# Kernel tuning notes

Hardware: AMD Instinct MI355X
Metric: run time of the kernel (lower is better)

## Reference

```python
import jax, jax.numpy as jnp
import numpy as np

D_MODEL = 2048
NUM_HEADS = 16
HEAD_DIM = D_MODEL // NUM_HEADS
BATCH = 2
SEQ = 2048


def setup_inputs() -> dict:
    key = jax.random.key(0)
    ks = jax.random.split(key, 5)
    s = 1.0 / np.sqrt(D_MODEL)
    return {
        "x": jax.random.normal(ks[0], (BATCH, SEQ, D_MODEL), dtype=jnp.float32),
        "Wq": jax.random.normal(ks[1], (D_MODEL, D_MODEL), dtype=jnp.float32) * s,
        "Wk": jax.random.normal(ks[2], (D_MODEL, D_MODEL), dtype=jnp.float32) * s,
        "Wv": jax.random.normal(ks[3], (D_MODEL, D_MODEL), dtype=jnp.float32) * s,
        "Wo": jax.random.normal(ks[4], (D_MODEL, D_MODEL), dtype=jnp.float32) * s,
    }


def reference(x, Wq, Wk, Wv, Wo):
    B, S, D = x.shape
    H, Dh = NUM_HEADS, HEAD_DIM
    # nn.Linear(bias=False): y = x @ W.T ; split_heads is a plain view (no transpose!)
    Q = (x @ Wq.T).reshape(B, H, S, Dh)
    K = (x @ Wk.T).reshape(B, H, S, Dh)
    V = (x @ Wv.T).reshape(B, H, S, Dh)
    # scores scaled by head_dim (NOT sqrt) — faithful to source
    scores = jnp.einsum("bhqd,bhkd->bhqk", Q, K) / jnp.float32(Dh)
    causal_mask = jnp.triu(jnp.ones((S, S), dtype=bool), k=1)  # True above diagonal
    scores = jnp.where(causal_mask, -jnp.inf, scores)
    attn = jax.nn.softmax(scores, axis=-1)
    out = jnp.einsum("bhqk,bhkd->bhqd", attn, V)  # [B,H,S,Dh]
    out = out.transpose(0, 2, 1, 3).reshape(B, S, D)  # merge DOES transpose
    return out @ Wo.T
```

## Files before the change

kernel.cpp:

```cpp
#include <hip/hip_runtime.h>
#include <hip/hip_bf16.h>

using bf16 = __hip_bfloat16;
typedef __attribute__((ext_vector_type(8))) short bf16x8;
typedef __attribute__((ext_vector_type(4))) float f32x4;

#define DEVI __device__ __forceinline__

constexpr int Bn = 2, Sn = 2048, Dn = 2048, Hn = 16, DHn = 128;
constexpr int Mn = Bn * Sn;

DEVI void gload_lds16(const bf16* g, bf16* l) {
  __builtin_amdgcn_global_load_lds(
      (__attribute__((address_space(1))) void*)g,
      (__attribute__((address_space(3))) void*)l,
      16, 0, 0);
}

__global__ __launch_bounds__(256) void cvt_all_k(const float* __restrict__ x,
                                                 const float* __restrict__ wq,
                                                 const float* __restrict__ wk,
                                                 const float* __restrict__ wv,
                                                 const float* __restrict__ wo,
                                                 bf16* __restrict__ xb,
                                                 bf16* __restrict__ wb) {
  const int which = blockIdx.y;
  const float* src;
  bf16* dst;
  int n8;
  if (which == 0) { src = x;  dst = xb; n8 = Mn * Dn / 8; }
  else {
    src = (which == 1) ? wq : (which == 2) ? wk : (which == 3) ? wv : wo;
    dst = wb + (size_t)(which - 1) * Dn * Dn;
    n8 = Dn * Dn / 8;
  }
  for (int i = blockIdx.x * 256 + threadIdx.x; i < n8; i += gridDim.x * 256) {
    const float4* p = (const float4*)src + (size_t)i * 2;
    float4 a = p[0], b = p[1];
    union { bf16 h[8]; bf16x8 v; } u;
    u.h[0] = __float2bfloat16(a.x); u.h[1] = __float2bfloat16(a.y);
    u.h[2] = __float2bfloat16(a.z); u.h[3] = __float2bfloat16(a.w);
    u.h[4] = __float2bfloat16(b.x); u.h[5] = __float2bfloat16(b.y);
    u.h[6] = __float2bfloat16(b.z); u.h[7] = __float2bfloat16(b.w);
    *((bf16x8*)dst + i) = u.v;
  }
}

template <int OUTF32, int NTOT, int NMAT, int MW>
__global__ __launch_bounds__(256, 2) void gemm3s(const bf16* __restrict__ A,
                                                 const bf16* __restrict__ W,
                                                 void* __restrict__ Cv) {
  constexpr int K = 2048, NT = K / 32;
  constexpr int BM = MW * 32;
  constexpr int SLOT = (BM + 128) * 32;
  __shared__ bf16 smem[3 * SLOT];

  constexpr int MT = Mn / BM;
  const int nwg = NTOT * MT;
  const int orig = blockIdx.x;
  const int wgid = (orig & 7) * (nwg >> 3) + (orig >> 3);
  const int bm = wgid / NTOT;
  const int bnn = wgid % NTOT;
  constexpr int nper = NTOT / NMAT;
  const int z = bnn / nper;
  const int col0 = (bnn % nper) * 128;

  const int t = threadIdx.x;
  const int wave = t >> 6, lane = t & 63;
  const int wm = wave >> 1, wn = wave & 1;
  const int lr = lane & 15, lg = lane >> 4;
  const int rch = ((lg ^ ((lr >> 1) & 3)) * 8);
  const int srow = t >> 2;
  const int sch = (t & 3) ^ ((t >> 3) & 3);

  const bf16* Ab = A + (size_t)(bm * BM + srow) * K + sch * 8;
  const bf16* Bb = W + (size_t)z * (2048 * 2048) +
                   (size_t)(col0 + srow) * K + sch * 8;

  auto stgA = [&](int slot, int kt, int u) {
    gload_lds16(Ab + (size_t)u * 64 * K + kt * 32,
                smem + slot * SLOT + u * 2048 + t * 8);
  };
  auto stgB = [&](int slot, int kt, int v) {
    gload_lds16(Bb + (size_t)v * 64 * K + kt * 32,
                smem + slot * SLOT + BM * 32 + v * 2048 + t * 8);
  };
  auto stage_tile = [&](int slot, int kt) {
#pragma unroll
    for (int u = 0; u < MW / 2; ++u) stgA(slot, kt, u);
    stgB(slot, kt, 0); stgB(slot, kt, 1);
  };

  f32x4 acc[MW][4];
  const f32x4 zf = {0.f, 0.f, 0.f, 0.f};
#pragma unroll
  for (int i = 0; i < MW; ++i)
#pragma unroll
    for (int j = 0; j < 4; ++j) acc[i][j] = zf;

  stage_tile(0, 0);
  stage_tile(1, 1);

  int slot = 0;
#pragma unroll 1
  for (int kt = 0; kt < NT; ++kt) {
    const bf16* sAb = smem + slot * SLOT;
    const bf16* sBb = sAb + BM * 32;

    if (kt == NT - 1)            asm volatile("s_waitcnt vmcnt(0)" ::: "memory");
    else if constexpr (MW == 8)  asm volatile("s_waitcnt vmcnt(6)" ::: "memory");
    else                         asm volatile("s_waitcnt vmcnt(4)" ::: "memory");
    __builtin_amdgcn_s_barrier();

    if (kt + 2 < NT) {
      int ps = slot + 2; if (ps >= 3) ps -= 3;
      stage_tile(ps, kt + 2);
    }

    bf16x8 bv[4], af[MW];
#pragma unroll
    for (int n = 0; n < 4; ++n)
      bv[n] = *(const bf16x8*)(sBb + (wn * 64 + n * 16 + lr) * 32 + rch);
#pragma unroll
    for (int i = 0; i < MW; ++i)
      af[i] = *(const bf16x8*)(sAb + (wm * (MW * 16) + i * 16 + lr) * 32 + rch);

    __builtin_amdgcn_s_setprio(1);
#pragma unroll
    for (int i = 0; i < MW; ++i)
#pragma unroll
      for (int n = 0; n < 4; ++n)
        acc[i][n] = __builtin_amdgcn_mfma_f32_16x16x32_bf16(af[i], bv[n], acc[i][n], 0, 0, 0);
    __builtin_amdgcn_s_setprio(0);

    slot = (slot == 2) ? 0 : slot + 1;
  }

  const int r0 = bm * BM + wm * (MW * 16), c0 = col0 + wn * 64;
#pragma unroll
  for (int mm = 0; mm < MW; ++mm)
#pragma unroll
    for (int nn = 0; nn < 4; ++nn) {
      const int rr = r0 + mm * 16 + lg * 4;
      const int cc = c0 + nn * 16 + lr;
#pragma unroll
      for (int r = 0; r < 4; ++r) {
        float v = acc[mm][nn][r];
        if (OUTF32) {
          ((float*)Cv)[(size_t)(rr + r) * 2048 + cc] = v;
        } else {
          bf16* C = (bf16*)Cv + (size_t)z * (Mn * 2048);
          C[(size_t)(rr + r) * 2048 + cc] = __float2bfloat16(v);
        }
      }
    }
}

__global__ __launch_bounds__(256, 2) void transpose_v(const bf16* __restrict__ V,
                                                      bf16* __restrict__ VT) {
  __shared__ bf16 tile[128 * 128];
  const int kt = blockIdx.x, bh = blockIdx.y;
  const bf16* Vh = V + (size_t)bh * (Sn * DHn);
  bf16* VTh = VT + (size_t)bh * (DHn * Sn);
  const int t = threadIdx.x;
  const int rr = t >> 4, cc = t & 15;
#pragma unroll
  for (int i = 0; i < 8; ++i) {
    int r = rr + i * 16;
    int ch = cc ^ ((r >> 3) & 7);
    *(bf16x8*)(tile + r * 128 + ch * 8) =
        *(const bf16x8*)(Vh + (size_t)(kt * 128 + r) * DHn + cc * 8);
  }
  __syncthreads();
  const int dr = t >> 4, li = t & 15;
#pragma unroll
  for (int i = 0; i < 8; ++i) {
    int dh = dr + i * 16;
    union { bf16 h[8]; bf16x8 v; } u;
#pragma unroll
    for (int j = 0; j < 8; ++j) {
      int k = li * 8 + j;
      int ch = (dh >> 3) ^ ((k >> 3) & 7);
      u.h[j] = tile[k * 128 + ch * 8 + (dh & 7)];
    }
    *(bf16x8*)(VTh + (size_t)dh * Sn + kt * 128 + li * 8) = u.v;
  }
}

__global__ __launch_bounds__(512, 1) void attn_k3(const bf16* __restrict__ Q,
                                                  const bf16* __restrict__ K,
                                                  const bf16* __restrict__ VT,
                                                  bf16* __restrict__ Mg) {
  __shared__ bf16 smem[40960];
  bf16* sK0 = smem;
  bf16* sK1 = smem + 8192;
  bf16* sV0 = smem + 16384;
  bf16* sV1 = smem + 24576;
  bf16* sP  = smem + 32768;
  bf16* sO  = smem;

  const int j = blockIdx.x;
  const int bh = blockIdx.y;
  const bf16* Qh = Q + (size_t)bh * (Sn * DHn);
  const bf16* Kh = K + (size_t)bh * (Sn * DHn);
  const bf16* VTh = VT + (size_t)bh * (DHn * Sn);
  const int b = bh >> 4, h = bh & 15;

  const int t = threadIdx.x, wave = t >> 6, lane = t & 63;
  const int lr = lane & 15, lg = lane >> 4;

  auto STAGE = [&](int buf, int kt) {
    bf16* dK = buf ? sK1 : sK0;
    bf16* dV = buf ? sV1 : sV0;
#pragma unroll
    for (int i = 0; i < 2; ++i) {
      int c = i * 512 + t;
      int row = c >> 4, c16 = c & 15;
      gload_lds16(Kh + (size_t)(kt * 64 + row) * DHn + ((c16 ^ (row & 7)) * 8),
                  dK + c * 8);
    }
#pragma unroll
    for (int i = 0; i < 2; ++i) {
      int c = i * 512 + t;
      int row = c >> 3, c8 = c & 7;
      gload_lds16(VTh + (size_t)row * Sn + kt * 64 + ((c8 ^ (row & 7)) * 8),
                  dV + c * 8);
    }
  };

  const f32x4 zf = {0.f, 0.f, 0.f, 0.f};

  for (int pi = 0; pi < 2; ++pi) {
    const int qb = pi ? (15 - j) : j;
    const int nt = qb * 2 + 2;
    const int q0 = qb * 128 + wave * 16;

    bf16x8 qf[4];
#pragma unroll
    for (int kk = 0; kk < 4; ++kk)
      qf[kk] = *(const bf16x8*)(Qh + (size_t)(q0 + lr) * DHn + kk * 32 + lg * 8);

    f32x4 o[8];
#pragma unroll
    for (int d = 0; d < 8; ++d) o[d] = zf;
    float mrun[4], lrun[4];
#pragma unroll
    for (int r = 0; r < 4; ++r) { mrun[r] = -3e38f; lrun[r] = 0.f; }

    STAGE(0, 0);
    __syncthreads();
    int cur = 0;

    for (int kt = 0; kt < nt; ++kt) {
      if (kt + 1 < nt) STAGE(cur ^ 1, kt + 1);

      bf16* sKc = cur ? sK1 : sK0;
      bf16* sVc = cur ? sV1 : sV0;

      f32x4 sfr[4];
#pragma unroll
      for (int nn = 0; nn < 4; ++nn) sfr[nn] = zf;
#pragma unroll
      for (int kk = 0; kk < 4; ++kk)
#pragma unroll
        for (int nn = 0; nn < 4; ++nn) {
          int row = nn * 16 + lr;
          int ch = (kk * 4 + lg) ^ (row & 7);
          bf16x8 kf = *(const bf16x8*)(sKc + row * DHn + ch * 8);
          sfr[nn] = __builtin_amdgcn_mfma_f32_16x16x32_bf16(qf[kk], kf, sfr[nn], 0, 0, 0);
        }

      const bool maskt = (kt >= qb * 2);
      float pv[4][4];
#pragma unroll
      for (int nn = 0; nn < 4; ++nn)
#pragma unroll
        for (int r = 0; r < 4; ++r) {
          float v = sfr[nn][r] * (1.0f / 128.0f);
          if (maskt) {
            int kg = kt * 64 + nn * 16 + lr;
            int qg = q0 + lg * 4 + r;
            if (kg > qg) v = -1e30f;
          }
          pv[nn][r] = v;
        }
      float mnew[4], alpha[4], rsum[4];
#pragma unroll
      for (int r = 0; r < 4; ++r) {
        float rm = fmaxf(fmaxf(pv[0][r], pv[1][r]), fmaxf(pv[2][r], pv[3][r]));
        rm = fmaxf(rm, __shfl_xor(rm, 1));
        rm = fmaxf(rm, __shfl_xor(rm, 2));
        rm = fmaxf(rm, __shfl_xor(rm, 4));
        rm = fmaxf(rm, __shfl_xor(rm, 8));
        mnew[r] = fmaxf(mrun[r], rm);
        alpha[r] = __expf(mrun[r] - mnew[r]);
        mrun[r] = mnew[r];
        rsum[r] = 0.f;
      }
#pragma unroll
      for (int nn = 0; nn < 4; ++nn)
#pragma unroll
        for (int r = 0; r < 4; ++r) {
          float p = __expf(pv[nn][r] - mnew[r]);
          pv[nn][r] = p;
          rsum[r] += p;
        }
#pragma unroll
      for (int r = 0; r < 4; ++r) {
        float s = rsum[r];
        s += __shfl_xor(s, 1); s += __shfl_xor(s, 2);
        s += __shfl_xor(s, 4); s += __shfl_xor(s, 8);
        lrun[r] = lrun[r] * alpha[r] + s;
      }
#pragma unroll
      for (int d = 0; d < 8; ++d)
#pragma unroll
        for (int r = 0; r < 4; ++r) o[d][r] *= alpha[r];

#pragma unroll
      for (int nn = 0; nn < 4; ++nn)
#pragma unroll
        for (int r = 0; r < 4; ++r) {
          int row = lg * 4 + r;
          int chk = (nn * 2 + (lr >> 3)) ^ (row & 7);
          sP[wave * 1024 + row * 64 + chk * 8 + (lr & 7)] = __float2bfloat16(pv[nn][r]);
        }

      bf16x8 pf[2];
#pragma unroll
      for (int kk = 0; kk < 2; ++kk) {
        int ch = (kk * 4 + lg) ^ (lr & 7);
        pf[kk] = *(const bf16x8*)(sP + wave * 1024 + lr * 64 + ch * 8);
      }
#pragma unroll
      for (int d = 0; d < 8; ++d)
#pragma unroll
        for (int kk = 0; kk < 2; ++kk) {
          int vrow = d * 16 + lr;
          int vch = (kk * 4 + lg) ^ (vrow & 7);
          bf16x8 vf = *(const bf16x8*)(sVc + vrow * 64 + vch * 8);
          o[d] = __builtin_amdgcn_mfma_f32_16x16x32_bf16(pf[kk], vf, o[d], 0, 0, 0);
        }

      __syncthreads();
      cur ^= 1;
    }

    float inv[4];
#pragma unroll
    for (int r = 0; r < 4; ++r) inv[r] = 1.0f / lrun[r];
#pragma unroll
    for (int d = 0; d < 8; ++d)
#pragma unroll
      for (int r = 0; r < 4; ++r) {
        int row = wave * 16 + lg * 4 + r;
        int col = d * 16 + lr;
        int chk = ((col >> 3) ^ (row & 7));
        sO[row * 128 + chk * 8 + (col & 7)] = __float2bfloat16(o[d][r] * inv[r]);
      }
    __syncthreads();
    bf16* Mh = Mg + ((size_t)(b * Sn + qb * 128)) * Dn + h * DHn;
#pragma unroll
    for (int i = 0; i < 4; ++i) {
      int row = (t >> 4) + i * 32;
      int c16 = t & 15;
      *(bf16x8*)(Mh + (size_t)row * Dn + c16 * 8) =
          *(const bf16x8*)(sO + row * 128 + ((c16 ^ (row & 7)) * 8));
    }
    __syncthreads();
  }
}

extern "C" void kernel_launch(void* const* d_in, const int* in_sizes, int n_in,
                              void* d_out, int out_size, void* d_ws, size_t ws_size,
                              hipStream_t stream) {
  const float* x = (const float*)d_in[0];
  const float* Wq = (const float*)d_in[1];
  const float* Wk = (const float*)d_in[2];
  const float* Wv = (const float*)d_in[3];
  const float* Wo = (const float*)d_in[4];
  float* out = (float*)d_out;

  char* ws = (char*)d_ws;
  bf16* xb = (bf16*)ws;            ws += (size_t)Mn * Dn * 2;
  bf16* Wb = (bf16*)ws;            ws += (size_t)4 * Dn * Dn * 2;
  bf16* QKV = (bf16*)ws;           ws += (size_t)3 * Mn * Dn * 2;
  bf16* VT = (bf16*)ws;            ws += (size_t)Bn * Hn * DHn * Sn * 2;
  bf16* Mg = (bf16*)ws;            ws += (size_t)Mn * Dn * 2;

  cvt_all_k<<<dim3(2048, 5), 256, 0, stream>>>(x, Wq, Wk, Wv, Wo, xb, Wb);

  gemm3s<0, 48, 3, 8><<<768, 256, 0, stream>>>(xb, Wb, (void*)QKV);

  transpose_v<<<dim3(16, 32), 256, 0, stream>>>(QKV + 2 * (size_t)Mn * Dn, VT);

  attn_k3<<<dim3(8, 32), 512, 0, stream>>>(QKV, QKV + (size_t)Mn * Dn, VT, Mg);

  gemm3s<1, 16, 1, 4><<<512, 256, 0, stream>>>(Mg, Wb + 3 * (size_t)Dn * Dn, (void*)out);
}
```

Before: 258.5 us.

## Replace GEMM with 8-wave 128x256 K64 tile kernel and remap attention blocks

```diff
diff --git a/kernel.cpp b/kernel.cpp
--- a/kernel.cpp
+++ b/kernel.cpp
@@ -46,99 +46,118 @@
   }
 }
 
-template <int OUTF32, int NTOT, int NMAT, int MW>
-__global__ __launch_bounds__(256, 2) void gemm3s(const bf16* __restrict__ A,
+template <int OUTF32, int NCT, int NMAT>
+__global__ __launch_bounds__(512, 1) void gemm8f(const bf16* __restrict__ A,
                                                  const bf16* __restrict__ W,
                                                  void* __restrict__ Cv) {
-  constexpr int K = 2048, NT = K / 32;
-  constexpr int BM = MW * 32;
-  constexpr int SLOT = (BM + 128) * 32;
-  __shared__ bf16 smem[3 * SLOT];
-
-  constexpr int MT = Mn / BM;
-  const int nwg = NTOT * MT;
+  constexpr int K = 2048, NT = K / 64;
+  constexpr int SLOTE = (128 + 256) * 64;
+  __shared__ bf16 smem[3 * SLOTE];
+
+  constexpr int MT = Mn / 128;
+  const int nwg = MT * NCT;
   const int orig = blockIdx.x;
   const int wgid = (orig & 7) * (nwg >> 3) + (orig >> 3);
-  const int bm = wgid / NTOT;
-  const int bnn = wgid % NTOT;
-  constexpr int nper = NTOT / NMAT;
-  const int z = bnn / nper;
-  const int col0 = (bnn % nper) * 128;
+  const int bm = wgid / NCT;
+  const int bcn = wgid % NCT;
+  constexpr int nper = NCT / NMAT;
+  const int z = bcn / nper;
+  const int col0 = (bcn % nper) * 256;
 
   const int t = threadIdx.x;
   const int wave = t >> 6, lane = t & 63;
-  const int wm = wave >> 1, wn = wave & 1;
+  const int wm = wave >> 2, wn = wave & 3;
   const int lr = lane & 15, lg = lane >> 4;
-  const int rch = ((lg ^ ((lr >> 1) & 3)) * 8);
-  const int srow = t >> 2;
-  const int sch = (t & 3) ^ ((t >> 3) & 3);
-
-  const bf16* Ab = A + (size_t)(bm * BM + srow) * K + sch * 8;
+  const int swz = lr & 7;
+
+  const int srow = t >> 3;
+  const int schk = (t & 7) ^ (srow & 7);
+  const bf16* Ab = A + (size_t)(bm * 128 + srow) * K + schk * 8;
   const bf16* Bb = W + (size_t)z * (2048 * 2048) +
-                   (size_t)(col0 + srow) * K + sch * 8;
+                   (size_t)(col0 + srow) * K + schk * 8;
 
   auto stgA = [&](int slot, int kt, int u) {
-    gload_lds16(Ab + (size_t)u * 64 * K + kt * 32,
-                smem + slot * SLOT + u * 2048 + t * 8);
+    gload_lds16(Ab + (size_t)u * 64 * K + kt * 64,
+                smem + slot * SLOTE + u * 4096 + t * 8);
   };
-  auto stgB = [&](int slot, int kt, int v) {
-    gload_lds16(Bb + (size_t)v * 64 * K + kt * 32,
-                smem + slot * SLOT + BM * 32 + v * 2048 + t * 8);
+  auto stgB = [&](int slot, int kt, int u) {
+    gload_lds16(Bb + (size_t)u * 64 * K + kt * 64,
+                smem + slot * SLOTE + 8192 + u * 4096 + t * 8);
   };
-  auto stage_tile = [&](int slot, int kt) {
-#pragma unroll
-    for (int u = 0; u < MW / 2; ++u) stgA(slot, kt, u);
-    stgB(slot, kt, 0); stgB(slot, kt, 1);
-  };
-
-  f32x4 acc[MW][4];
+
+  f32x4 acc[4][4];
   const f32x4 zf = {0.f, 0.f, 0.f, 0.f};
 #pragma unroll
-  for (int i = 0; i < MW; ++i)
+  for (int i = 0; i < 4; ++i)
 #pragma unroll
     for (int j = 0; j < 4; ++j) acc[i][j] = zf;
 
-  stage_tile(0, 0);
-  stage_tile(1, 1);
-
-  int slot = 0;
+  stgA(0, 0, 0); stgA(0, 0, 1);
+  stgB(0, 0, 0); stgB(0, 0, 1); stgB(0, 0, 2); stgB(0, 0, 3);
+  stgA(1, 1, 0); stgA(1, 1, 1);
+  stgB(1, 1, 0); stgB(1, 1, 1); stgB(1, 1, 2); stgB(1, 1, 3);
+
+  int sl = 0;
 #pragma unroll 1
   for (int kt = 0; kt < NT; ++kt) {
-    const bf16* sAb = smem + slot * SLOT;
-    const bf16* sBb = sAb + BM * 32;
-
-    if (kt == NT - 1)            asm volatile("s_waitcnt vmcnt(0)" ::: "memory");
-    else if constexpr (MW == 8)  asm volatile("s_waitcnt vmcnt(6)" ::: "memory");
-    else                         asm volatile("s_waitcnt vmcnt(4)" ::: "memory");
+    const bf16* sA = smem + sl * SLOTE;
+    const bf16* sB = sA + 8192;
+    int sl2 = sl + 2; if (sl2 >= 3) sl2 -= 3;
+    const bool pf = (kt + 2 < NT);
+
+    if (kt == NT - 1) asm volatile("s_waitcnt vmcnt(0)" ::: "memory");
+    else              asm volatile("s_waitcnt vmcnt(6)" ::: "memory");
     __builtin_amdgcn_s_barrier();
 
-    if (kt + 2 < NT) {
-      int ps = slot + 2; if (ps >= 3) ps -= 3;
-      stage_tile(ps, kt + 2);
-    }
-
-    bf16x8 bv[4], af[MW];
-#pragma unroll
-    for (int n = 0; n < 4; ++n)
-      bv[n] = *(const bf16x8*)(sBb + (wn * 64 + n * 16 + lr) * 32 + rch);
-#pragma unroll
-    for (int i = 0; i < MW; ++i)
-      af[i] = *(const bf16x8*)(sAb + (wm * (MW * 16) + i * 16 + lr) * 32 + rch);
-
-    __builtin_amdgcn_s_setprio(1);
-#pragma unroll
-    for (int i = 0; i < MW; ++i)
+    {
+      bf16x8 af[4], bv[4];
+#pragma unroll
+      for (int i = 0; i < 4; ++i)
+        af[i] = *(const bf16x8*)(sA + (wm * 64 + i * 16 + lr) * 64 + ((lg ^ swz) * 8));
 #pragma unroll
       for (int n = 0; n < 4; ++n)
-        acc[i][n] = __builtin_amdgcn_mfma_f32_16x16x32_bf16(af[i], bv[n], acc[i][n], 0, 0, 0);
-    __builtin_amdgcn_s_setprio(0);
-
-    slot = (slot == 2) ? 0 : slot + 1;
-  }
-
-  const int r0 = bm * BM + wm * (MW * 16), c0 = col0 + wn * 64;
-#pragma unroll
-  for (int mm = 0; mm < MW; ++mm)
+        bv[n] = *(const bf16x8*)(sB + (wn * 64 + n * 16 + lr) * 64 + ((lg ^ swz) * 8));
+      if (pf) { stgA(sl2, kt + 2, 0); stgA(sl2, kt + 2, 1); stgB(sl2, kt + 2, 0); }
+      __builtin_amdgcn_s_barrier();
+      asm volatile("s_waitcnt lgkmcnt(0)" ::: "memory");
+      __builtin_amdgcn_sched_barrier(0);
+      __builtin_amdgcn_s_setprio(1);
+#pragma unroll
+      for (int i = 0; i < 4; ++i)
+#pragma unroll
+        for (int n = 0; n < 4; ++n)
+          acc[i][n] = __builtin_amdgcn_mfma_f32_16x16x32_bf16(af[i], bv[n], acc[i][n], 0, 0, 0);
+      __builtin_amdgcn_s_setprio(0);
+      __builtin_amdgcn_s_barrier();
+    }
+
+    {
+      bf16x8 af[4], bv[4];
+#pragma unroll
+      for (int i = 0; i < 4; ++i)
+        af[i] = *(const bf16x8*)(sA + (wm * 64 + i * 16 + lr) * 64 + (((4 + lg) ^ swz) * 8));
+#pragma unroll
+      for (int n = 0; n < 4; ++n)
+        bv[n] = *(const bf16x8*)(sB + (wn * 64 + n * 16 + lr) * 64 + (((4 + lg) ^ swz) * 8));
+      if (pf) { stgB(sl2, kt + 2, 1); stgB(sl2, kt + 2, 2); stgB(sl2, kt + 2, 3); }
+      __builtin_amdgcn_s_barrier();
+      asm volatile("s_waitcnt lgkmcnt(0)" ::: "memory");
+      __builtin_amdgcn_sched_barrier(0);
+      __builtin_amdgcn_s_setprio(1);
+#pragma unroll
+      for (int i = 0; i < 4; ++i)
+#pragma unroll
+        for (int n = 0; n < 4; ++n)
+          acc[i][n] = __builtin_amdgcn_mfma_f32_16x16x32_bf16(af[i], bv[n], acc[i][n], 0, 0, 0);
+      __builtin_amdgcn_s_setprio(0);
+    }
+
+    sl = (sl == 2) ? 0 : sl + 1;
+  }
+
+  const int r0 = bm * 128 + wm * 64, c0 = col0 + wn * 64;
+#pragma unroll
+  for (int mm = 0; mm < 4; ++mm)
 #pragma unroll
     for (int nn = 0; nn < 4; ++nn) {
       const int rr = r0 + mm * 16 + lg * 4;
@@ -199,8 +218,10 @@
   bf16* sP  = smem + 32768;
   bf16* sO  = smem;
 
-  const int j = blockIdx.x;
-  const int bh = blockIdx.y;
+  const int bi = blockIdx.x;
+  const int xcd = bi & 7, slt = bi >> 3;
+  const int bh = (slt & 3) * 8 + xcd;
+  const int j = slt >> 2;
   const bf16* Qh = Q + (size_t)bh * (Sn * DHn);
   const bf16* Kh = K + (size_t)bh * (Sn * DHn);
   const bf16* VTh = VT + (size_t)bh * (DHn * Sn);
@@ -390,11 +411,11 @@
 
   cvt_all_k<<<dim3(2048, 5), 256, 0, stream>>>(x, Wq, Wk, Wv, Wo, xb, Wb);
 
-  gemm3s<0, 48, 3, 8><<<768, 256, 0, stream>>>(xb, Wb, (void*)QKV);
+  gemm8f<0, 24, 3><<<768, 512, 0, stream>>>(xb, Wb, (void*)QKV);
 
   transpose_v<<<dim3(16, 32), 256, 0, stream>>>(QKV + 2 * (size_t)Mn * Dn, VT);
 
-  attn_k3<<<dim3(8, 32), 512, 0, stream>>>(QKV, QKV + (size_t)Mn * Dn, VT, Mg);
-
-  gemm3s<1, 16, 1, 4><<<512, 256, 0, stream>>>(Mg, Wb + 3 * (size_t)Dn * Dn, (void*)out);
-}
+  attn_k3<<<256, 512, 0, stream>>>(QKV, QKV + (size_t)Mn * Dn, VT, Mg);
+
+  gemm8f<1, 8, 1><<<256, 512, 0, stream>>>(Mg, Wb + 3 * (size_t)Dn * Dn, (void*)out);
+}
```

Measured after the change: 257.0 us. No clear change (-0.6%).
